# Kernel optimization log

Hardware: AMD Instinct MI355X
Metric: run time of the kernel (lower is better)

The kernel has to match this reference:

```python
import jax, jax.numpy as jnp
import numpy as np

B, T, C = 4, 1024, 1024
HEAD_SIZE = 64
H = C // HEAD_SIZE
N_LAYER, LAYER_ID = 24, 12
D_MIX_LORA, D_DECAY_LORA = 32, 64
HEAD_SIZE_DIVISOR = 8
LN_EPS = 1e-5 * HEAD_SIZE_DIVISOR ** 2


def setup_inputs() -> dict:
    key = jax.random.key(0)
    ks = jax.random.split(key, 16)
    x = jax.random.normal(ks[0], (B, T, C), jnp.float32)

    r01 = LAYER_ID / (N_LAYER - 1)          # ratio_0_to_1
    r10 = 1.0 - LAYER_ID / N_LAYER          # ratio_1_to_almost0
    ddd = np.arange(C, dtype=np.float64) / C

    time_maa_x = jnp.asarray((1.0 - ddd ** r10).astype(np.float32))
    time_maa_w = jnp.asarray((1.0 - ddd ** r10).astype(np.float32))
    time_maa_k = jnp.asarray((1.0 - ddd ** r10).astype(np.float32))
    time_maa_v = jnp.asarray((1.0 - (ddd ** r10 + 0.3 * r01)).astype(np.float32))
    time_maa_r = jnp.asarray((1.0 - ddd ** (0.5 * r10)).astype(np.float32))
    time_maa_g = jnp.asarray((1.0 - ddd ** (0.5 * r10)).astype(np.float32))

    n = np.arange(C, dtype=np.float64)
    time_decay = jnp.asarray((-6.0 + 5.0 * (n / (C - 1)) ** (0.7 + 1.3 * r01)).astype(np.float32))
    zigzag = ((n + 1) % 3 - 1) * 0.1
    time_faaaa = jnp.asarray((r01 * (1.0 - n / (C - 1)) + zigzag).astype(np.float32)).reshape(H, HEAD_SIZE)

    u = lambda k, shp: jax.random.uniform(k, shp, jnp.float32, -0.01, 0.01)
    time_maa_w1 = u(ks[1], (C, D_MIX_LORA * 5))   # zeros in orig init; small random for a non-trivial test
    time_maa_w2 = u(ks[2], (5, D_MIX_LORA, C))
    time_decay_w1 = u(ks[3], (C, D_DECAY_LORA))
    time_decay_w2 = u(ks[4], (D_DECAY_LORA, C))

    s = 1.0 / np.sqrt(C)
    Wr = jax.random.normal(ks[5], (C, C), jnp.float32) * s   # stored [in, out]
    Wk = jax.random.normal(ks[6], (C, C), jnp.float32) * s
    Wv = jax.random.normal(ks[7], (C, C), jnp.float32) * s
    Wg = jax.random.normal(ks[8], (C, C), jnp.float32) * s
    Wo = jax.random.normal(ks[9], (C, C), jnp.float32) * s
    ln_w = jnp.ones((C,), jnp.float32)
    ln_b = jnp.zeros((C,), jnp.float32)

    return dict(x=x, time_maa_x=time_maa_x, time_maa_w=time_maa_w, time_maa_k=time_maa_k,
                time_maa_v=time_maa_v, time_maa_r=time_maa_r, time_maa_g=time_maa_g,
                time_maa_w1=time_maa_w1, time_maa_w2=time_maa_w2,
                time_decay=time_decay, time_decay_w1=time_decay_w1, time_decay_w2=time_decay_w2,
                time_faaaa=time_faaaa, Wr=Wr, Wk=Wk, Wv=Wv, Wg=Wg, Wo=Wo, ln_w=ln_w, ln_b=ln_b)


def _wkv6(r, k, v, w, u):
    # r,k,v,w: [B,T,H,N]; u: [H,N]. Data-dependent linear recurrence per head.
    def step(S, inp):               # S: [B,H,N,N] (key dim j, value dim i)
        r_t, k_t, v_t, w_t = inp    # each [B,H,N]
        y = jnp.einsum('bhj,bhji->bhi', r_t, S) \
            + jnp.sum(r_t * u * k_t, axis=-1, keepdims=True) * v_t
        decay = jnp.exp(-jnp.exp(w_t))            # CUDA kernel: w_eff = exp(-exp(w))
        S = decay[..., None] * S + k_t[..., None] * v_t[..., None, :]
        return S, y

    to_t = lambda a: jnp.transpose(a, (1, 0, 2, 3))  # [T,B,H,N]
    S0 = jnp.zeros(r.shape[:1] + (r.shape[2], r.shape[3], r.shape[3]), r.dtype)
    _, ys = jax.lax.scan(step, S0, (to_t(r), to_t(k), to_t(v), to_t(w)))
    return jnp.transpose(ys, (1, 0, 2, 3))            # [B,T,H,N]


def reference(x, time_maa_x, time_maa_w, time_maa_k, time_maa_v, time_maa_r, time_maa_g,
              time_maa_w1, time_maa_w2, time_decay, time_decay_w1, time_decay_w2,
              time_faaaa, Wr, Wk, Wv, Wg, Wo, ln_w, ln_b):
    b, t, c = x.shape
    h, n = H, HEAD_SIZE

    # token shift: ZeroPad2d((0,0,1,-1)) shifts time right by one with zero pad
    xx = jnp.concatenate([jnp.zeros_like(x[:, :1]), x[:, :-1]], axis=1) - x
    xxx = x + xx * time_maa_x
    mix = jnp.tanh(xxx @ time_maa_w1).reshape(b, t, 5, D_MIX_LORA)
    m = jnp.einsum('btsd,sdc->sbtc', mix, time_maa_w2)  # [5,B,T,C]
    xw = x + xx * (time_maa_w + m[0])
    xk = x + xx * (time_maa_k + m[1])
    xv = x + xx * (time_maa_v + m[2])
    xr = x + xx * (time_maa_r + m[3])
    xg = x + xx * (time_maa_g + m[4])

    r = xr @ Wr
    k = xk @ Wk
    v = xv @ Wv
    g = jax.nn.silu(xg @ Wg)
    w = time_decay + jnp.tanh(xw @ time_decay_w1) @ time_decay_w2

    y = _wkv6(r.reshape(b, t, h, n), k.reshape(b, t, h, n),
              v.reshape(b, t, h, n), w.reshape(b, t, h, n), time_faaaa)

    # GroupNorm with n_head groups over channel dim, eps = 1e-5 * divisor^2
    mu = y.mean(-1, keepdims=True)
    var = y.var(-1, keepdims=True)
    yn = ((y - mu) / jnp.sqrt(var + LN_EPS)).reshape(b, t, c) * ln_w + ln_b

    return (yn * g) @ Wo
```

## Files before the change

kernel.cpp:

```cpp
#include <hip/hip_runtime.h>

typedef unsigned short u16;
typedef short short8 __attribute__((ext_vector_type(8)));
typedef short short4v __attribute__((ext_vector_type(4)));
typedef float float4v __attribute__((ext_vector_type(4)));
typedef float float2v __attribute__((ext_vector_type(2)));
typedef unsigned uint4v __attribute__((ext_vector_type(4)));

__device__ __forceinline__ float bf2f(u16 h) { return __uint_as_float(((unsigned)h) << 16); }
__device__ __forceinline__ u16 f2bf(float f) {
  unsigned u = __float_as_uint(f);
  unsigned r = (u + 0x7fffu + ((u >> 16) & 1u)) >> 16;
  return (u16)r;
}
__device__ __forceinline__ bool is_f32(const void* probe) {
  return ((const u16*)probe)[0] != 0x3F80;
}
__device__ __forceinline__ float ldin(const void* p, long i, bool f32m) {
  return f32m ? ((const float*)p)[i] : bf2f(((const u16*)p)[i]);
}

typedef __attribute__((address_space(1))) const unsigned int as1_u32;
typedef __attribute__((address_space(3))) unsigned int as3_u32;
__device__ __forceinline__ void gl2lds16(const void* g, void* l) {
  __builtin_amdgcn_global_load_lds((as1_u32*)g, (as3_u32*)l, 16, 0, 0);
}

template <int CTRL>
__device__ __forceinline__ float dpp_add(float x) {
  int s = __builtin_amdgcn_update_dpp(0, __float_as_int(x), CTRL, 0xF, 0xF, true);
  return x + __int_as_float(s);
}

__global__ __launch_bounds__(256) void sentinel_fill(u16* o, long n) {
  long i = (long)blockIdx.x * 256 + threadIdx.x;
  if (i < n) o[i] = 0x42C8;
}

struct TDescArr {
  const void* src[13];
  u16* dst[13];
  int rows[13];
  int cols[13];
  int roff[13];
};

__global__ __launch_bounds__(256) void transpose_all(TDescArr d, const void* probe) {
  bool f32m = is_f32(probe);
  int z = blockIdx.z;
  int rows = d.rows[z], cols = d.cols[z], roff = d.roff[z];
  int bc = blockIdx.x * 32, br = blockIdx.y * 32;
  if (bc >= cols || br >= rows) return;
  const void* src = d.src[z];
  u16* dst = d.dst[z];
  __shared__ u16 tile[32][33];
  int tx = threadIdx.x & 31, ty = threadIdx.x >> 5;
#pragma unroll
  for (int i = 0; i < 32; i += 8)
    tile[ty + i][tx] = f2bf(ldin(src, (long)(roff + br + ty + i) * cols + bc + tx, f32m));
  __syncthreads();
#pragma unroll
  for (int i = 0; i < 32; i += 8)
    dst[(long)(bc + ty + i) * rows + br + tx] = tile[tx][ty + i];
}

__global__ __launch_bounds__(256) void token_shift(const void* __restrict__ x,
                                                   const void* __restrict__ maa_x,
                                                   u16* __restrict__ xxx) {
  bool f32m = is_f32(maa_x);
  long idx = (long)blockIdx.x * 256 + threadIdx.x;
  int c = (int)(idx & 1023);
  int tt = (int)((idx >> 10) & 1023);
  float xv = ldin(x, idx, f32m);
  float xp = tt > 0 ? ldin(x, idx - 1024, f32m) : 0.f;
  xxx[idx] = f2bf(xv + (xp - xv) * ldin(maa_x, c, f32m));
}

template <int EPI>
__device__ __forceinline__ void gemm128_core(const u16* __restrict__ A,
                                             const u16* __restrict__ Bt,
                                             void* __restrict__ Cv, int N, int K,
                                             int m0, int n0, u16* As, u16* Bs,
                                             bool f32m) {
  int t = threadIdx.x, lane = t & 63, w = t >> 6;
  int wm = (w >> 1) * 64, wn = (w & 1) * 64;
  int lr = lane & 15, lk = lane >> 4;
  float4v acc[4][4];
#pragma unroll
  for (int i = 0; i < 4; i++)
#pragma unroll
    for (int j = 0; j < 4; j++) acc[i][j] = (float4v){0.f, 0.f, 0.f, 0.f};
  int srow = t >> 3;
  int scol = ((t & 7) ^ (srow & 7)) * 8;
  const u16* Ag = A + (long)(m0 + srow) * K + scol;
  const u16* Bg = Bt + (long)(n0 + srow) * K + scol;
  int so = w * 512;
  for (int k0 = 0; k0 < K; k0 += 64) {
    __syncthreads();
#pragma unroll
    for (int p = 0; p < 4; p++) {
      gl2lds16(Ag + (long)p * 32 * K + k0, As + p * 2048 + so);
      gl2lds16(Bg + (long)p * 32 * K + k0, Bs + p * 2048 + so);
    }
    __syncthreads();
    short8 af[4][2], bfr[4][2];
#pragma unroll
    for (int i = 0; i < 4; i++) {
      int R = wm + i * 16 + lr;
#pragma unroll
      for (int h = 0; h < 2; h++) {
        int j = h * 4 + lk;
        af[i][h] = *(const short8*)(As + R * 64 + (j ^ (R & 7)) * 8);
      }
    }
#pragma unroll
    for (int i = 0; i < 4; i++) {
      int R = wn + i * 16 + lr;
#pragma unroll
      for (int h = 0; h < 2; h++) {
        int j = h * 4 + lk;
        bfr[i][h] = *(const short8*)(Bs + R * 64 + (j ^ (R & 7)) * 8);
      }
    }
#pragma unroll
    for (int mi2 = 0; mi2 < 4; mi2++)
#pragma unroll
      for (int ni2 = 0; ni2 < 4; ni2++) {
        acc[mi2][ni2] = __builtin_amdgcn_mfma_f32_16x16x32_bf16(
            af[mi2][0], bfr[ni2][0], acc[mi2][ni2], 0, 0, 0);
        acc[mi2][ni2] = __builtin_amdgcn_mfma_f32_16x16x32_bf16(
            af[mi2][1], bfr[ni2][1], acc[mi2][ni2], 0, 0, 0);
      }
  }
#pragma unroll
  for (int mi2 = 0; mi2 < 4; mi2++) {
#pragma unroll
    for (int ni2 = 0; ni2 < 4; ni2++) {
      int col = n0 + wn + ni2 * 16 + lr;
#pragma unroll
      for (int rr = 0; rr < 4; rr++) {
        long row = m0 + wm + mi2 * 16 + lk * 4 + rr;
        float val = acc[mi2][ni2][rr];
        if (EPI == 1) val = val / (1.f + __expf(-val));
        if (EPI == 2 && f32m) ((float*)Cv)[row * N + col] = val;
        else ((u16*)Cv)[row * N + col] = f2bf(val);
      }
    }
  }
}

template <int EPI>
__global__ __launch_bounds__(256, 2) void gemm_big(const u16* __restrict__ A,
                                                   const u16* __restrict__ Bt,
                                                   void* __restrict__ Cv, int M, int N,
                                                   int K, const void* probe) {
  __shared__ alignas(16) u16 As[128 * 64];
  __shared__ alignas(16) u16 Bs[128 * 64];
  int sid = blockIdx.y * gridDim.x + blockIdx.x;
  int per8 = (gridDim.x * gridDim.y) >> 3;
  int L = (sid & 7) * per8 + (sid >> 3);
  int mi = L / gridDim.y, ni = L % gridDim.y;
  bool f32m = (EPI == 2) ? is_f32(probe) : false;
  gemm128_core<EPI>(A, Bt, Cv, N, K, mi * 128, ni * 128, As, Bs, f32m);
}

template <int EPI0, int EPI1>
__global__ __launch_bounds__(256, 2) void gemm_big2(
    const u16* __restrict__ A0, const u16* __restrict__ Bt0, u16* __restrict__ C0,
    const u16* __restrict__ A1, const u16* __restrict__ Bt1, u16* __restrict__ C1,
    int M, int N, int K) {
  __shared__ alignas(16) u16 As[128 * 64];
  __shared__ alignas(16) u16 Bs[128 * 64];
  int z = blockIdx.z;
  int sid = blockIdx.y * gridDim.x + blockIdx.x;
  int per8 = (gridDim.x * gridDim.y) >> 3;
  int L = (sid & 7) * per8 + (sid >> 3);
  int mi = L / gridDim.y, ni = L % gridDim.y;
  if (z == 0)
    gemm128_core<EPI0>(A0, Bt0, C0, N, K, mi * 128, ni * 128, As, Bs, false);
  else
    gemm128_core<EPI1>(A1, Bt1, C1, N, K, mi * 128, ni * 128, As, Bs, false);
}

template <int EPI>
__global__ __launch_bounds__(256) void gemm_wave(const u16* __restrict__ A, int lda,
                                                 const u16* __restrict__ Bt,
                                                 u16* __restrict__ C, int ldc,
                                                 float* dA_, float* dB_, int Ntot,
                                                 int K, const void* aux0,
                                                 const void* probe,
                                                 const void* __restrict__ xin) {
  int t = threadIdx.x, lane = t & 63, w = t >> 6;
  int m0 = blockIdx.x * 64 + w * 16;
  int span = Ntot / gridDim.y;
  int col0 = blockIdx.y * span;
  const u16* Bp = Bt + (long)col0 * K;
  int lr = lane & 15, lk = lane >> 4;
  bool f32m = (EPI >= 2) ? is_f32(probe) : false;
  int nt = span >> 4;
  for (int g0 = 0; g0 < nt; g0 += 4) {
    int gc = (nt - g0 < 4) ? (nt - g0) : 4;
    float4v acc[4];
#pragma unroll
    for (int i = 0; i < 4; i++) acc[i] = (float4v){0.f, 0.f, 0.f, 0.f};
    for (int k0 = 0; k0 < K; k0 += 32) {
      short8 a = *(const short8*)(A + (long)(m0 + lr) * lda + k0 + lk * 8);
      for (int gi = 0; gi < gc; gi++) {
        int n0 = (g0 + gi) * 16;
        short8 b = *(const short8*)(Bp + (long)(n0 + lr) * K + k0 + lk * 8);
        acc[gi] = __builtin_amdgcn_mfma_f32_16x16x32_bf16(a, b, acc[gi], 0, 0, 0);
      }
    }
    for (int gi = 0; gi < gc; gi++) {
      int col = col0 + (g0 + gi) * 16 + lr;
      if (EPI == 3) {
        long r0 = m0 + lk * 4;
        float xv4[4];
#pragma unroll
        for (int rr = 0; rr < 4; rr++)
          xv4[rr] = ldin(xin, (r0 + rr) * 1024 + col, f32m);
        float xpv = ((int)(r0 & 1023) > 0) ? ldin(xin, (r0 - 1) * 1024 + col, f32m) : 0.f;
        float mv = ldin(aux0, col, f32m);
#pragma unroll
        for (int rr = 0; rr < 4; rr++) {
          float xv = xv4[rr];
          float xp = (rr == 0) ? xpv : xv4[rr - 1];
          C[(r0 + rr) * 1024 + col] = f2bf(xv + (xp - xv) * (mv + acc[gi][rr]));
        }
      } else {
#pragma unroll
        for (int rr = 0; rr < 4; rr++) {
          long row = m0 + lk * 4 + rr;
          float val = acc[gi][rr];
          if (EPI == 0) {
            C[row * ldc + col] = f2bf(val);
          } else if (EPI == 1) {
            float vv = fminf(fmaxf(val, -15.f), 15.f);
            float e = __expf(2.f * vv);
            C[row * ldc + col] = f2bf((e - 1.f) / (e + 1.f));
          } else if (EPI == 2) {
            float wv = val + ldin(aux0, col, f32m);
            float dv = __expf(-__expf(wv));
            if (row < 2048) dA_[row * 1024 + col] = dv;
            else dB_[(row - 2048) * 1024 + col] = dv;
          }
        }
      }
    }
  }
}

__global__ __launch_bounds__(256) void gemm_wave3_pair(
    const u16* __restrict__ A0, const u16* __restrict__ Bt0, u16* __restrict__ C0,
    const void* __restrict__ maa0, const u16* __restrict__ A1,
    const u16* __restrict__ Bt1, u16* __restrict__ C1,
    const void* __restrict__ maa1, const void* probe,
    const void* __restrict__ xin) {
  int z = blockIdx.z;
  const u16* A = z ? A1 : A0;
  const u16* Bt = z ? Bt1 : Bt0;
  u16* C = z ? C1 : C0;
  const void* maa = z ? maa1 : maa0;
  bool f32m = is_f32(probe);
  int t = threadIdx.x, lane = t & 63, w = t >> 6;
  int m0 = blockIdx.x * 64 + w * 16;
  int col0 = blockIdx.y * 32;
  const u16* Bp = Bt + (long)col0 * 32;
  int lr = lane & 15, lk = lane >> 4;
  float4v acc[2];
  acc[0] = (float4v){0.f, 0.f, 0.f, 0.f};
  acc[1] = (float4v){0.f, 0.f, 0.f, 0.f};
  short8 a = *(const short8*)(A + (long)(m0 + lr) * 160 + lk * 8);
#pragma unroll
  for (int gi = 0; gi < 2; gi++) {
    short8 b = *(const short8*)(Bp + (long)(gi * 16 + lr) * 32 + lk * 8);
    acc[gi] = __builtin_amdgcn_mfma_f32_16x16x32_bf16(a, b, acc[gi], 0, 0, 0);
  }
#pragma unroll
  for (int gi = 0; gi < 2; gi++) {
    int col = col0 + gi * 16 + lr;
    long r0 = m0 + lk * 4;
    float xv4[4];
#pragma unroll
    for (int rr = 0; rr < 4; rr++)
      xv4[rr] = ldin(xin, (r0 + rr) * 1024 + col, f32m);
    float xpv = ((int)(r0 & 1023) > 0) ? ldin(xin, (r0 - 1) * 1024 + col, f32m) : 0.f;
    float mv = ldin(maa, col, f32m);
#pragma unroll
    for (int rr = 0; rr < 4; rr++) {
      float xv = xv4[rr];
      float xp = (rr == 0) ? xpv : xv4[rr - 1];
      C[(r0 + rr) * 1024 + col] = f2bf(xv + (xp - xv) * (mv + acc[gi][rr]));
    }
  }
}

__global__ __launch_bounds__(256) void gemm_n64_tanh(const u16* __restrict__ A,
                                                     const u16* __restrict__ Bt,
                                                     u16* __restrict__ C) {
  int t = threadIdx.x, lane = t & 63, w = t >> 6;
  int m0 = blockIdx.x * 16;
  int n0 = w * 16;
  int lr = lane & 15, lk = lane >> 4;
  float4v acc = (float4v){0.f, 0.f, 0.f, 0.f};
  const u16* Ap = A + (long)(m0 + lr) * 1024;
  const u16* Bp = Bt + (long)(n0 + lr) * 1024;
  for (int k0 = 0; k0 < 1024; k0 += 32) {
    short8 a = *(const short8*)(Ap + k0 + lk * 8);
    short8 b = *(const short8*)(Bp + k0 + lk * 8);
    acc = __builtin_amdgcn_mfma_f32_16x16x32_bf16(a, b, acc, 0, 0, 0);
  }
#pragma unroll
  for (int rr = 0; rr < 4; rr++) {
    long row = m0 + lk * 4 + rr;
    float vv = fminf(fmaxf(acc[rr], -15.f), 15.f);
    float e = __expf(2.f * vv);
    C[row * 64 + n0 + lr] = f2bf((e - 1.f) / (e + 1.f));
  }
}

__global__ __launch_bounds__(256) void wkv6_kernel(
    const u16* __restrict__ r, const u16* __restrict__ k, const u16* __restrict__ v,
    const float* __restrict__ dA_, const float* __restrict__ dB_,
    const void* __restrict__ u_, const void* probe, u16* __restrict__ y) {
  bool f32m = is_f32(probe);
  int bx = blockIdx.x;
  int cb = bx >> 6, bh = bx & 63;
  int b = bh >> 4, h = bh & 15;
  int t = threadIdx.x, lane = t & 63, w = t >> 6;
  int cl = lane >> 3, jq = lane & 7;
  int kp = w * 8 + jq;
  __shared__ alignas(16) uint4v rkd[32][33];
  __shared__ alignas(16) float vsm[8][36];
  __shared__ alignas(16) float ypn[4][8][36];
  float2v S = (float2v){0.f, 0.f};
  float2v u2;
  u2[0] = ldin(u_, h * 64 + 2 * kp, f32m);
  u2[1] = ldin(u_, h * 64 + 2 * kp + 1, f32m);
  const long base = ((long)b << 20) + h * 64;
  const float* dgb =
      (b < 2 ? dA_ + (long)b * 1048576 : dB_ + (long)(b - 2) * 1048576) + h * 64;

  int s_tt = t >> 5, s_kp = t & 31;
  int v_tt = t >> 3, v_c = t & 7;

  for (int c0 = 0; c0 < 1024; c0 += 32) {
    {
#pragma unroll
      for (int i = 0; i < 4; i++) {
        int tt = s_tt + i * 8;
        long ro = (long)(c0 + tt) << 10;
        unsigned r2 = *(const unsigned*)(r + base + ro + s_kp * 2);
        unsigned k2 = *(const unsigned*)(k + base + ro + s_kp * 2);
        const float* dp = dgb + ro + s_kp * 2;
        rkd[tt][s_kp] =
            (uint4v){r2, k2, __float_as_uint(dp[0]), __float_as_uint(dp[1])};
      }
      vsm[v_c][v_tt] = bf2f(v[base + ((long)(c0 + v_tt) << 10) + cb * 8 + v_c]);
    }
    __syncthreads();
    float4v vv4;
    float4v yy4;
#pragma unroll
    for (int tt = 0; tt < 32; ++tt) {
      if ((tt & 3) == 0) vv4 = *(const float4v*)&vsm[cl][tt];
      float vt = vv4[tt & 3];
      uint4v q = rkd[tt][kp];
      float2v rv, kv2, dv;
      rv[0] = __uint_as_float(q[0] << 16);
      rv[1] = __uint_as_float(q[0] & 0xffff0000u);
      kv2[0] = __uint_as_float(q[1] << 16);
      kv2[1] = __uint_as_float(q[1] & 0xffff0000u);
      dv[0] = __uint_as_float(q[2]);
      dv[1] = __uint_as_float(q[3]);
      float2v vt2 = (float2v){vt, vt};
      float2v kv = kv2 * vt2;
      float2v y2 = rv * (u2 * kv + S);
      S = S * dv + kv;
      float yy = y2[0] + y2[1];
      yy = dpp_add<0xB1>(yy);
      yy = dpp_add<0x4E>(yy);
      yy = dpp_add<0x104>(yy);
      yy4[tt & 3] = yy;
      if ((tt & 3) == 3 && jq == 0)
        *(float4v*)&ypn[w][cl][tt - 3] = yy4;
    }
    __syncthreads();
    {
      int rt = t >> 3, rc = t & 7;
      float s = (ypn[0][rc][rt] + ypn[1][rc][rt]) + (ypn[2][rc][rt] + ypn[3][rc][rt]);
      y[base + ((long)(c0 + rt) << 10) + cb * 8 + rc] = f2bf(s);
    }
    __syncthreads();
  }
}

__global__ __launch_bounds__(256) void gn_gate(const u16* __restrict__ y,
                                               const u16* __restrict__ g,
                                               const void* __restrict__ lnw,
                                               const void* __restrict__ lnb,
                                               const void* probe,
                                               u16* __restrict__ out) {
  bool f32m = is_f32(probe);
  int gid = blockIdx.x * 4 + (threadIdx.x >> 6);
  int lane = threadIdx.x & 63;
  int h = gid & 15;
  long row = gid >> 4;
  long off = row * 1024 + h * 64 + lane;
  float val = bf2f(y[off]);
  float s = val, sq = val * val;
#pragma unroll
  for (int m = 1; m < 64; m <<= 1) {
    s += __shfl_xor(s, m);
    sq += __shfl_xor(sq, m);
  }
  float mean = s * (1.f / 64.f);
  float var = fmaxf(sq * (1.f / 64.f) - mean * mean, 0.f);
  float inv = rsqrtf(var + 6.4e-4f);
  int c = h * 64 + lane;
  float yn = (val - mean) * inv * ldin(lnw, c, f32m) + ldin(lnb, c, f32m);
  out[off] = f2bf(yn * bf2f(g[off]));
}

extern "C" void kernel_launch(void* const* d_in, const int* in_sizes, int n_in,
                              void* d_out, int out_size, void* d_ws, size_t ws_size,
                              hipStream_t stream) {
  const void* x = d_in[0];
  const void* maaX = d_in[1];
  const void* maa_s[5] = {d_in[2], d_in[3], d_in[4], d_in[5], d_in[6]};
  const void* w1 = d_in[7];
  const void* w2 = d_in[8];
  const void* tdec = d_in[9];
  const void* dw1 = d_in[10];
  const void* dw2 = d_in[11];
  const void* faaaa = d_in[12];
  const void* Wr = d_in[13];
  const void* Wk = d_in[14];
  const void* Wv = d_in[15];
  const void* Wg = d_in[16];
  const void* Wo = d_in[17];
  const void* lnw = d_in[18];
  const void* lnb = d_in[19];

  const long oWoT = 4194304;
  const long ow1T = 5242880;
  const long odw1T = 5406720;
  const long odw2T = 5472256;
  const long ow2T = 5537792;
  const long omixb = 5701632;
  const long owtan = 6356992;
  const long oxxxg = 6619136;
  const long omx = 10813440;
  const long orb = 15007744;
  const long okb = 19202048;
  const long ovb = 23396352;
  const long oyb = 27590656;
  const long oend = 31784960;
  const size_t needed = (size_t)oend * 2;

  if (ws_size < needed) {
    sentinel_fill<<<dim3((unsigned)((out_size + 255) / 256)), 256, 0, stream>>>(
        (u16*)d_out, out_size);
    return;
  }

  u16* W = (u16*)d_ws;
  u16* WrT = W;
  u16* WkT = W + 1048576;
  u16* WvT = W + 2097152;
  u16* WgT = W + 3145728;
  u16* WoT = W + oWoT;
  u16* w1T = W + ow1T;
  u16* dw1T = W + odw1T;
  u16* dw2T = W + odw2T;
  u16* w2T = W + ow2T;
  u16* mixb = W + omixb;
  u16* wtan = W + owtan;
  u16* xxxg = W + oxxxg;
  u16* mx = W + omx;
  u16* rbuf = W + orb;
  u16* kbuf = W + okb;
  u16* vbuf = W + ovb;
  u16* ybuf = W + oyb;
  float* dA_ = (float*)W;
  float* dB_ = (float*)(W + omx);
  u16* gated = mx;

  TDescArr td;
  const void* s5[5] = {Wr, Wk, Wv, Wg, Wo};
  u16* t5[5] = {WrT, WkT, WvT, WgT, WoT};
  for (int i = 0; i < 13; i++) td.roff[i] = 0;
  for (int i = 0; i < 5; i++) {
    td.src[i] = s5[i]; td.dst[i] = t5[i]; td.rows[i] = 1024; td.cols[i] = 1024;
  }
  td.src[5] = w1;  td.dst[5] = w1T;  td.rows[5] = 1024; td.cols[5] = 160;
  td.src[6] = dw1; td.dst[6] = dw1T; td.rows[6] = 1024; td.cols[6] = 64;
  td.src[7] = dw2; td.dst[7] = dw2T; td.rows[7] = 64;   td.cols[7] = 1024;
  for (int s = 0; s < 5; s++) {
    td.src[8 + s] = w2;
    td.dst[8 + s] = w2T + s * 1024 * 32;
    td.rows[8 + s] = 32; td.cols[8 + s] = 1024; td.roff[8 + s] = s * 32;
  }

  transpose_all<<<dim3(32, 32, 13), 256, 0, stream>>>(td, maaX);
  token_shift<<<dim3(16384), 256, 0, stream>>>(x, maaX, xxxg);
  gemm_wave<1><<<dim3(64, 10), 256, 0, stream>>>(xxxg, 1024, w1T, mixb, 160, nullptr,
                                                 nullptr, 160, 1024, nullptr, nullptr,
                                                 nullptr);
  gemm_wave3_pair<<<dim3(64, 32, 2), 256, 0, stream>>>(
      mixb + 3 * 32, w2T + 3 * 32768, mx, maa_s[3],
      mixb + 1 * 32, w2T + 1 * 32768, ybuf, maa_s[1], maaX, x);
  gemm_big2<0, 0><<<dim3(32, 8, 2), 256, 0, stream>>>(mx, WrT, rbuf, ybuf, WkT, kbuf,
                                                      4096, 1024, 1024);
  gemm_wave3_pair<<<dim3(64, 32, 2), 256, 0, stream>>>(
      mixb + 2 * 32, w2T + 2 * 32768, mx, maa_s[2],
      mixb + 4 * 32, w2T + 4 * 32768, ybuf, maa_s[4], maaX, x);
  gemm_big2<0, 1><<<dim3(32, 8, 2), 256, 0, stream>>>(mx, WvT, vbuf, ybuf, WgT, xxxg,
                                                      4096, 1024, 1024);
  gemm_wave<3><<<dim3(64, 32), 256, 0, stream>>>(mixb + 0 * 32, 160, w2T + 0 * 32768,
                                                 mx, 1024, nullptr, nullptr, 1024, 32,
                                                 maa_s[0], maaX, x);
  gemm_n64_tanh<<<dim3(256), 256, 0, stream>>>(mx, dw1T, wtan);
  gemm_wave<2><<<dim3(64, 16), 256, 0, stream>>>(wtan, 64, dw2T, nullptr, 0, dA_, dB_,
                                                 1024, 64, tdec, maaX, nullptr);
  wkv6_kernel<<<dim3(512), 256, 0, stream>>>(rbuf, kbuf, vbuf, dA_, dB_, faaaa, maaX,
                                             ybuf);
  gn_gate<<<dim3(16384), 256, 0, stream>>>(ybuf, xxxg, lnw, lnb, maaX, gated);
  gemm_big<2><<<dim3(32, 8), 256, 0, stream>>>(gated, WoT, d_out, 4096, 1024, 1024, maaX);
}
```

Before: 378.0 us.

## Replace sequential WKV6 recurrence with chunked MFMA formulation using cumulative log-decay

```diff
diff --git a/kernel.cpp b/kernel.cpp
--- a/kernel.cpp
+++ b/kernel.cpp
@@ -4,7 +4,6 @@
 typedef short short8 __attribute__((ext_vector_type(8)));
 typedef short short4v __attribute__((ext_vector_type(4)));
 typedef float float4v __attribute__((ext_vector_type(4)));
-typedef float float2v __attribute__((ext_vector_type(2)));
 typedef unsigned uint4v __attribute__((ext_vector_type(4)));
 
 __device__ __forceinline__ float bf2f(u16 h) { return __uint_as_float(((unsigned)h) << 16); }
@@ -240,9 +239,9 @@
             C[row * ldc + col] = f2bf((e - 1.f) / (e + 1.f));
           } else if (EPI == 2) {
             float wv = val + ldin(aux0, col, f32m);
-            float dv = __expf(-__expf(wv));
-            if (row < 2048) dA_[row * 1024 + col] = dv;
-            else dB_[(row - 2048) * 1024 + col] = dv;
+            float ew = __expf(wv);
+            if (row < 2048) dA_[row * 1024 + col] = ew;
+            else dB_[(row - 2048) * 1024 + col] = ew;
           }
         }
       }
@@ -319,79 +318,152 @@
   }
 }
 
-__global__ __launch_bounds__(256) void wkv6_kernel(
+__global__ __launch_bounds__(256) void wkv6_chunk(
     const u16* __restrict__ r, const u16* __restrict__ k, const u16* __restrict__ v,
-    const float* __restrict__ dA_, const float* __restrict__ dB_,
+    const float* __restrict__ ewA, const float* __restrict__ ewB,
     const void* __restrict__ u_, const void* probe, u16* __restrict__ y) {
   bool f32m = is_f32(probe);
   int bx = blockIdx.x;
-  int cb = bx >> 6, bh = bx & 63;
+  int vs = bx & 1, bh = bx >> 1;
   int b = bh >> 4, h = bh & 15;
-  int t = threadIdx.x, lane = t & 63, w = t >> 6;
-  int cl = lane >> 3, jq = lane & 7;
-  int kp = w * 8 + jq;
-  __shared__ alignas(16) uint4v rkd[32][33];
-  __shared__ alignas(16) float vsm[8][36];
-  __shared__ alignas(16) float ypn[4][8][36];
-  float2v S = (float2v){0.f, 0.f};
-  float2v u2;
-  u2[0] = ldin(u_, h * 64 + 2 * kp, f32m);
-  u2[1] = ldin(u_, h * 64 + 2 * kp + 1, f32m);
+  int tid = threadIdx.x, lane = tid & 63, w = tid >> 6;
+  int lr = lane & 15, lk = lane >> 4;
+
+  __shared__ alignas(16) float sc[32][68];
+  __shared__ alignas(16) u16 Rp[32][72];
+  __shared__ alignas(16) u16 Kp[32][72];
+  __shared__ alignas(16) u16 Kd[64][40];
+  __shared__ alignas(16) u16 Vt[32][40];
+  __shared__ alignas(16) u16 Pb[32][40];
+  __shared__ alignas(16) u16 Sh[32][72];
+  __shared__ alignas(16) u16 Sl[32][72];
+  __shared__ float diag32[32];
+
   const long base = ((long)b << 20) + h * 64;
-  const float* dgb =
-      (b < 2 ? dA_ + (long)b * 1048576 : dB_ + (long)(b - 2) * 1048576) + h * 64;
-
-  int s_tt = t >> 5, s_kp = t & 31;
-  int v_tt = t >> 3, v_c = t & 7;
+  const float* ewg =
+      (b < 2 ? ewA + (long)b * 1048576 : ewB + (long)(b - 2) * 1048576) + h * 64;
+
+  int tt = tid >> 3, kg = tid & 7;
+  float u8[8];
+#pragma unroll
+  for (int i = 0; i < 8; i++) u8[i] = ldin(u_, h * 64 + kg * 8 + i, f32m);
+
+  float4v Sst[2];
+  Sst[0] = (float4v){0.f, 0.f, 0.f, 0.f};
+  Sst[1] = (float4v){0.f, 0.f, 0.f, 0.f};
+  int skey = w * 16 + lk * 4;
 
   for (int c0 = 0; c0 < 1024; c0 += 32) {
-    {
-#pragma unroll
-      for (int i = 0; i < 4; i++) {
-        int tt = s_tt + i * 8;
-        long ro = (long)(c0 + tt) << 10;
-        unsigned r2 = *(const unsigned*)(r + base + ro + s_kp * 2);
-        unsigned k2 = *(const unsigned*)(k + base + ro + s_kp * 2);
-        const float* dp = dgb + ro + s_kp * 2;
-        rkd[tt][s_kp] =
-            (uint4v){r2, k2, __float_as_uint(dp[0]), __float_as_uint(dp[1])};
-      }
-      vsm[v_c][v_tt] = bf2f(v[base + ((long)(c0 + v_tt) << 10) + cb * 8 + v_c]);
-    }
+    long grow = (long)(c0 + tt) << 10;
+    float4v ewlo = *(const float4v*)(ewg + grow + kg * 8);
+    float4v ewhi = *(const float4v*)(ewg + grow + kg * 8 + 4);
+    short8 rraw = *(const short8*)(r + base + grow + kg * 8);
+    short8 kraw = *(const short8*)(k + base + grow + kg * 8);
+    short4v vraw = *(const short4v*)(v + base + grow + vs * 32 + kg * 4);
     __syncthreads();
-    float4v vv4;
-    float4v yy4;
-#pragma unroll
-    for (int tt = 0; tt < 32; ++tt) {
-      if ((tt & 3) == 0) vv4 = *(const float4v*)&vsm[cl][tt];
-      float vt = vv4[tt & 3];
-      uint4v q = rkd[tt][kp];
-      float2v rv, kv2, dv;
-      rv[0] = __uint_as_float(q[0] << 16);
-      rv[1] = __uint_as_float(q[0] & 0xffff0000u);
-      kv2[0] = __uint_as_float(q[1] << 16);
-      kv2[1] = __uint_as_float(q[1] & 0xffff0000u);
-      dv[0] = __uint_as_float(q[2]);
-      dv[1] = __uint_as_float(q[3]);
-      float2v vt2 = (float2v){vt, vt};
-      float2v kv = kv2 * vt2;
-      float2v y2 = rv * (u2 * kv + S);
-      S = S * dv + kv;
-      float yy = y2[0] + y2[1];
-      yy = dpp_add<0xB1>(yy);
-      yy = dpp_add<0x4E>(yy);
-      yy = dpp_add<0x104>(yy);
-      yy4[tt & 3] = yy;
-      if ((tt & 3) == 3 && jq == 0)
-        *(float4v*)&ypn[w][cl][tt - 3] = yy4;
+    *(float4v*)&sc[tt][kg * 8] = ewlo;
+    *(float4v*)&sc[tt][kg * 8 + 4] = ewhi;
+#pragma unroll
+    for (int i = 0; i < 4; i++) Vt[kg * 4 + i][tt] = (u16)vraw[i];
+#pragma unroll
+    for (int vt = 0; vt < 2; vt++) {
+      short4v hi4, lo4;
+#pragma unroll
+      for (int rr = 0; rr < 4; rr++) {
+        u16 hv = f2bf(Sst[vt][rr]);
+        hi4[rr] = (short)hv;
+        lo4[rr] = (short)f2bf(Sst[vt][rr] - bf2f(hv));
+      }
+      *(short4v*)&Sh[lr + vt * 16][skey] = hi4;
+      *(short4v*)&Sl[lr + vt * 16][skey] = lo4;
+    }
+    __syncthreads();
+    if (tid < 64) {
+      float s = 0.f;
+#pragma unroll
+      for (int t2 = 0; t2 < 32; t2++) {
+        s += sc[t2][tid];
+        sc[t2][tid] = s;
+      }
     }
     __syncthreads();
     {
-      int rt = t >> 3, rc = t & 7;
-      float s = (ypn[0][rc][rt] + ypn[1][rc][rt]) + (ypn[2][rc][rt] + ypn[3][rc][rt]);
-      y[base + ((long)(c0 + rt) << 10) + cb * 8 + rc] = f2bf(s);
+      float pd = 0.f;
+      short8 rpv, kpv;
+#pragma unroll
+      for (int i = 0; i < 8; i++) {
+        int key = kg * 8 + i;
+        float rf = bf2f((u16)rraw[i]);
+        float kf = bf2f((u16)kraw[i]);
+        float si = sc[tt][key];
+        float sx = tt ? sc[tt - 1][key] : 0.f;
+        float sE = sc[31][key];
+        rpv[i] = (short)f2bf(rf * __expf(-sx));
+        kpv[i] = (short)f2bf(kf * __expf(si));
+        Kd[key][tt] = f2bf(kf * __expf(si - sE));
+        pd = fmaf(rf * u8[i], kf, pd);
+      }
+      *(short8*)&Rp[tt][kg * 8] = rpv;
+      *(short8*)&Kp[tt][kg * 8] = kpv;
+      pd = dpp_add<0xB1>(pd);
+      pd = dpp_add<0x4E>(pd);
+      pd = dpp_add<0x104>(pd);
+      if (kg == 0) diag32[tt] = pd;
     }
     __syncthreads();
+    {
+      int pt = w >> 1, pj = w & 1;
+      float4v pacc = (float4v){0.f, 0.f, 0.f, 0.f};
+      short8 aP0 = *(const short8*)&Rp[pt * 16 + lr][lk * 8];
+      short8 aP1 = *(const short8*)&Rp[pt * 16 + lr][lk * 8 + 32];
+      short8 bP0 = *(const short8*)&Kp[pj * 16 + lr][lk * 8];
+      short8 bP1 = *(const short8*)&Kp[pj * 16 + lr][lk * 8 + 32];
+      pacc = __builtin_amdgcn_mfma_f32_16x16x32_bf16(aP0, bP0, pacc, 0, 0, 0);
+      pacc = __builtin_amdgcn_mfma_f32_16x16x32_bf16(aP1, bP1, pacc, 0, 0, 0);
+      int jcol = pj * 16 + lr;
+#pragma unroll
+      for (int rr = 0; rr < 4; rr++) {
+        int trow = pt * 16 + lk * 4 + rr;
+        float val = (jcol < trow) ? pacc[rr] : (jcol == trow ? diag32[trow] : 0.f);
+        Pb[trow][jcol] = f2bf(val);
+      }
+    }
+    __syncthreads();
+    {
+      int yt = w >> 1, yv = w & 1;
+      float4v yacc = (float4v){0.f, 0.f, 0.f, 0.f};
+      short8 aY = *(const short8*)&Pb[yt * 16 + lr][lk * 8];
+      short8 bY = *(const short8*)&Vt[yv * 16 + lr][lk * 8];
+      yacc = __builtin_amdgcn_mfma_f32_16x16x32_bf16(aY, bY, yacc, 0, 0, 0);
+      short8 aR0 = *(const short8*)&Rp[yt * 16 + lr][lk * 8];
+      short8 aR1 = *(const short8*)&Rp[yt * 16 + lr][lk * 8 + 32];
+      short8 bH0 = *(const short8*)&Sh[yv * 16 + lr][lk * 8];
+      short8 bH1 = *(const short8*)&Sh[yv * 16 + lr][lk * 8 + 32];
+      short8 bL0 = *(const short8*)&Sl[yv * 16 + lr][lk * 8];
+      short8 bL1 = *(const short8*)&Sl[yv * 16 + lr][lk * 8 + 32];
+      yacc = __builtin_amdgcn_mfma_f32_16x16x32_bf16(aR0, bH0, yacc, 0, 0, 0);
+      yacc = __builtin_amdgcn_mfma_f32_16x16x32_bf16(aR1, bH1, yacc, 0, 0, 0);
+      yacc = __builtin_amdgcn_mfma_f32_16x16x32_bf16(aR0, bL0, yacc, 0, 0, 0);
+      yacc = __builtin_amdgcn_mfma_f32_16x16x32_bf16(aR1, bL1, yacc, 0, 0, 0);
+#pragma unroll
+      for (int rr = 0; rr < 4; rr++) {
+        int trow = yt * 16 + lk * 4 + rr;
+        y[base + ((long)(c0 + trow) << 10) + vs * 32 + yv * 16 + lr] = f2bf(yacc[rr]);
+      }
+      short8 aS = *(const short8*)&Kd[w * 16 + lr][lk * 8];
+      short8 bS0 = *(const short8*)&Vt[lr][lk * 8];
+      short8 bS1 = *(const short8*)&Vt[16 + lr][lk * 8];
+      float4v sa0 = (float4v){0.f, 0.f, 0.f, 0.f};
+      float4v sa1 = (float4v){0.f, 0.f, 0.f, 0.f};
+      sa0 = __builtin_amdgcn_mfma_f32_16x16x32_bf16(aS, bS0, sa0, 0, 0, 0);
+      sa1 = __builtin_amdgcn_mfma_f32_16x16x32_bf16(aS, bS1, sa1, 0, 0, 0);
+#pragma unroll
+      for (int rr = 0; rr < 4; rr++) {
+        float cl = __expf(-sc[31][skey + rr]);
+        Sst[0][rr] = fmaf(Sst[0][rr], cl, sa0[rr]);
+        Sst[1][rr] = fmaf(Sst[1][rr], cl, sa1[rr]);
+      }
+    }
   }
 }
 
@@ -523,8 +595,8 @@
   gemm_n64_tanh<<<dim3(256), 256, 0, stream>>>(mx, dw1T, wtan);
   gemm_wave<2><<<dim3(64, 16), 256, 0, stream>>>(wtan, 64, dw2T, nullptr, 0, dA_, dB_,
                                                  1024, 64, tdec, maaX, nullptr);
-  wkv6_kernel<<<dim3(512), 256, 0, stream>>>(rbuf, kbuf, vbuf, dA_, dB_, faaaa, maaX,
-                                             ybuf);
+  wkv6_chunk<<<dim3(128), 256, 0, stream>>>(rbuf, kbuf, vbuf, dA_, dB_, faaaa, maaX,
+                                            ybuf);
   gn_gate<<<dim3(16384), 256, 0, stream>>>(ybuf, xxxg, lnw, lnb, maaX, gated);
   gemm_big<2><<<dim3(32, 8), 256, 0, stream>>>(gated, WoT, d_out, 4096, 1024, 1024, maaX);
 }
```

Result: faster. 364.8 us (-3.5%).
